# Kernel tuning notes

Measured on AMD Instinct MI355X. Metric: run time of the kernel, lower is better.

Reference implementation:

```python
import jax, jax.numpy as jnp
import numpy as np
from jax.experimental.jet import jet
from jax.experimental.ode import odeint

STATE = 4096
CDIM = 1024
TAY_REG = 2


def sol_recursive(order, f, z, t):
    """Higher-order derivatives of the ODE dynamics via Taylor-mode (jet)."""
    if order < 2:
        return f(z, t), jnp.zeros_like(z)
    z_shape = z.shape
    z_t = jnp.concatenate((jnp.ravel(z), jnp.array([t], dtype=z.dtype)))

    def g(z_t):
        zz, tt = jnp.reshape(z_t[:-1], z_shape), z_t[-1]
        dz = jnp.ravel(f(zz, tt))
        dt = jnp.array([1.0], dtype=z_t.dtype)
        return jnp.concatenate((dz, dt))

    y0, yns = jet(g, (z_t,), ((jnp.ones_like(z_t),),))
    for _ in range(order - 1):
        y0, yns = jet(g, (z_t,), ((y0, *yns),))
    return jnp.reshape(y0[:-1], z_shape), jnp.reshape(yns[-2][:-1], z_shape)


def augment_dynamics(reg, dynamics):
    def aug_dynamics(yr, t):
        y, r = yr
        dydt, dy_r = sol_recursive(reg, dynamics, y, t)
        return dydt, jnp.mean(dy_r ** 2)[None] * jnp.ones(1, y.dtype) if False else (dydt, jnp.mean(dy_r ** 2) * jnp.ones(1, y.dtype))
    # flatten conditional artifact: redefine cleanly
    def aug(yr, t):
        y, r = yr
        dydt, dy_r = sol_recursive(reg, dynamics, y, t)
        return dydt, jnp.mean(dy_r ** 2) * jnp.ones(1, y.dtype)
    return aug


def setup_inputs() -> dict:
    key = jax.random.key(0)
    ks = jax.random.split(key, 5)
    fan_in = CDIM + STATE + 1
    s = 0.5 / np.sqrt(fan_in)  # tame Lipschitz constant -> modest adaptive step count
    h = jax.random.normal(ks[0], (STATE,), dtype=jnp.float32)
    c = jax.random.normal(ks[1], (CDIM,), dtype=jnp.float32)
    t = jnp.float32(1.0)
    W1 = jax.random.normal(ks[2], (fan_in, STATE), dtype=jnp.float32) * s
    b1 = jnp.zeros((STATE,), dtype=jnp.float32)
    W2 = jax.random.normal(ks[3], (fan_in, STATE), dtype=jnp.float32) * s
    b2 = jnp.zeros((STATE,), dtype=jnp.float32)
    return {"h": h, "t": t, "c": c, "W1": W1, "b1": b1, "W2": W2, "b2": b2}


def reference(h, t, c, W1, b1, W2, b2):
    # MLPDynamics: sigmoid(h) -> hstack(c, ., t) -> lin1 -> sigmoid -> hstack(c, ., t) -> lin2
    def dyn(hh, tt):
        out = jax.nn.sigmoid(hh)
        x = jnp.hstack((c, out, tt))          # [CDIM+STATE+1]
        out = jax.nn.sigmoid(x @ W1 + b1)     # [STATE]
        x2 = jnp.hstack((c, out, tt))
        return x2 @ W2 + b2                   # [STATE]

    aug = augment_dynamics(TAY_REG, dyn)
    ts = jnp.stack([jnp.zeros_like(t), t])
    ys, rs = odeint(aug, (h, jnp.zeros(1, h.dtype)), ts)
    # jnp.split(., 2)[1].squeeze() over the 2-row time axis == take row 1
    h1 = ys[1]
    r1 = rs[1].squeeze()
    return (h1, r1)
```

## Files before the change

kernel.cpp:

```cpp
#include <hip/hip_runtime.h>

#define N      4096
#define NROWS  4097
#define NC     1024
#define STEPS  4
#define TPB    256

typedef unsigned short us8 __attribute__((ext_vector_type(8)));

__device__ __forceinline__ float bf2f(unsigned short u) {
  union { unsigned int i; float f; } v; v.i = ((unsigned int)u) << 16; return v.f;
}
__device__ __forceinline__ unsigned short f2bf(float f) {
  union { float f; unsigned int i; } v; v.f = f;
  const unsigned int u = v.i;
  return (unsigned short)((u + 0x7FFFu + ((u >> 16) & 1u)) >> 16);
}
__device__ __forceinline__ float sigf(float x) { return 1.0f / (1.0f + __expf(-x)); }

__global__ __launch_bounds__(TPB) void k_init(const float* __restrict__ h,
                                              const float* __restrict__ b1,
                                              const float* __restrict__ b2,
                                              float* __restrict__ ycur,
                                              float* __restrict__ cp1,
                                              float* __restrict__ cp2,
                                              float* __restrict__ rk) {
  const int j = blockIdx.x * TPB + threadIdx.x;
  if (j < N) { ycur[j] = h[j]; cp1[j] = b1[j]; cp2[j] = b2[j]; }
  if (j < 16) rk[j] = 0.f;
}

__global__ __launch_bounds__(TPB) void k_conv(const float* __restrict__ W1,
                                              const float* __restrict__ W2,
                                              unsigned short* __restrict__ W1bf,
                                              unsigned short* __restrict__ W2bf) {
  const int row = blockIdx.x;
  const float* __restrict__ src = (blockIdx.y ? W2 : W1) + (size_t)(NC + row) * N;
  unsigned short* __restrict__ dst = (blockIdx.y ? W2bf : W1bf) + (size_t)row * N;
#pragma unroll
  for (int it = 0; it < 2; ++it) {
    const int col = it * 2048 + threadIdx.x * 8;
    const float4 a = *reinterpret_cast<const float4*>(src + col);
    const float4 b = *reinterpret_cast<const float4*>(src + col + 4);
    us8 o;
    o[0] = f2bf(a.x); o[1] = f2bf(a.y); o[2] = f2bf(a.z); o[3] = f2bf(a.w);
    o[4] = f2bf(b.x); o[5] = f2bf(b.y); o[6] = f2bf(b.z); o[7] = f2bf(b.w);
    *reinterpret_cast<us8*>(dst + col) = o;
  }
}

__global__ __launch_bounds__(TPB) void k_cpart(const float* __restrict__ W1,
                                               const float* __restrict__ W2,
                                               const float* __restrict__ c,
                                               float* __restrict__ cp1,
                                               float* __restrict__ cp2) {
  const float* __restrict__ W = blockIdx.z ? W2 : W1;
  float* __restrict__ cp = blockIdx.z ? cp2 : cp1;
  __shared__ float xs[128];
  __shared__ float red[8][256];
  const int tid = threadIdx.x;
  const int cb = blockIdx.x, rc = blockIdx.y;
  const int r0 = rc * 128;
  if (tid < 128) xs[tid] = c[r0 + tid];
  __syncthreads();
  const int cg = tid & 31, rg = tid >> 5;
  const float* __restrict__ wbase = W + (size_t)r0 * N + cb * 256 + cg * 8;
  float a[8] = {0,0,0,0,0,0,0,0};
#pragma unroll
  for (int k = 0; k < 16; ++k) {
    const int r = rg + (k << 3);
    const float xv = xs[r];
    const float4 wa = *reinterpret_cast<const float4*>(wbase + (size_t)r * N);
    const float4 wb = *reinterpret_cast<const float4*>(wbase + (size_t)r * N + 4);
    a[0] = fmaf(wa.x, xv, a[0]); a[1] = fmaf(wa.y, xv, a[1]);
    a[2] = fmaf(wa.z, xv, a[2]); a[3] = fmaf(wa.w, xv, a[3]);
    a[4] = fmaf(wb.x, xv, a[4]); a[5] = fmaf(wb.y, xv, a[5]);
    a[6] = fmaf(wb.z, xv, a[6]); a[7] = fmaf(wb.w, xv, a[7]);
  }
#pragma unroll
  for (int e = 0; e < 8; ++e) red[rg][cg * 8 + e] = a[e];
  __syncthreads();
  float ssum = 0.f;
#pragma unroll
  for (int g = 0; g < 8; ++g) ssum += red[g][tid];
  atomicAdd(&cp[cb * 256 + tid], ssum);
}

__global__ __launch_bounds__(TPB) void k_phase(
    int mode,
    const unsigned short* __restrict__ Wbf,
    const float* __restrict__ part_in,
    float* __restrict__ part_out,
    const float* __restrict__ cpart,
    const float* __restrict__ tptr,
    float* __restrict__ u1,
    float* __restrict__ fcur,
    const float* __restrict__ fprev,
    float* __restrict__ ycur,
    float* __restrict__ ksum,
    float* __restrict__ rk,
    int rkIdx, int s, float csv, float tmul, float tadd) {
  __shared__ float xs[128];
  __shared__ float red[8][256];
  const int tid = threadIdx.x;
  const int cb = blockIdx.x, rc = blockIdx.y;
  const int j0 = rc * 128;
  const float dtv = tptr[0] * (1.0f / STEPS);

  if (tid < 128) {
    const int j = j0 + tid;
    float xv;
    if (mode == 0) {
      xv = sigf(ycur[j]);
    } else {
      float ssum = 0.f;
#pragma unroll 8
      for (int r = 0; r < 32; ++r) ssum += part_in[(r << 12) + j];
      if (mode == 1) {
        const float u = ssum + cpart[j];
        if (cb == 0) u1[j] = u;
        xv = sigf(u);
      } else if (mode == 2) {
        const float fv = ssum + cpart[j];
        if (cb == 0) fcur[j] = fv;
        float ys = ycur[j];
        if (csv != 0.f) ys = fmaf(csv * dtv, fprev[j], ys);
        const float s0 = sigf(ys);
        xv = s0 * (1.f - s0) * fv;
      } else if (mode == 3) {
        if (cb == 0) {
          const float fc = fcur[j];
          if (s == 0)      ksum[j] = fc;
          else if (s < 3)  ksum[j] = fmaf(2.f, fc, ksum[j]);
          else             ycur[j] = fmaf(dtv * (1.f / 6.f), ksum[j] + fc, ycur[j]);
        }
        const float s1 = sigf(u1[j]);
        xv = s1 * (1.f - s1) * ssum;
      } else {
        float v = ssum * ssum;
#pragma unroll
        for (int off = 32; off >= 1; off >>= 1) v += __shfl_down(v, off);
        if (cb == 0 && (tid & 63) == 0) atomicAdd(&rk[rkIdx], v);
        float ys = ycur[j];
        if (csv != 0.f) ys = fmaf(csv * dtv, fprev[j], ys);
        xv = sigf(ys);
      }
    }
    xs[tid] = xv;
  }
  __syncthreads();

  const int cg = tid & 31, rg = tid >> 5;
  const unsigned short* __restrict__ wbase =
      Wbf + (size_t)j0 * N + cb * 256 + cg * 8;
  float a[8] = {0,0,0,0,0,0,0,0};
#pragma unroll
  for (int k = 0; k < 16; ++k) {
    const int r = rg + (k << 3);
    const float xv = xs[r];
    const us8 w = *reinterpret_cast<const us8*>(wbase + (size_t)r * N);
#pragma unroll
    for (int e = 0; e < 8; ++e) a[e] = fmaf(bf2f(w[e]), xv, a[e]);
  }
  if (rc == 31 && rg == 0) {
    const float coef = fmaf(tmul, dtv, tadd);
    const us8 w = *reinterpret_cast<const us8*>(
        Wbf + (size_t)N * N + cb * 256 + cg * 8);
#pragma unroll
    for (int e = 0; e < 8; ++e) a[e] = fmaf(bf2f(w[e]), coef, a[e]);
  }
#pragma unroll
  for (int e = 0; e < 8; ++e) red[rg][cg * 8 + e] = a[e];
  __syncthreads();
  float ssum = 0.f;
#pragma unroll
  for (int g = 0; g < 8; ++g) ssum += red[g][tid];
  part_out[(rc << 12) + cb * 256 + tid] = ssum;
}

__global__ __launch_bounds__(128) void k_last(const float* __restrict__ part_in,
                                              const float* __restrict__ ycur,
                                              float* __restrict__ rk,
                                              float* __restrict__ out) {
  const int tid = threadIdx.x;
  const int j = blockIdx.x * 128 + tid;
  float df = 0.f;
#pragma unroll 8
  for (int r = 0; r < 32; ++r) df += part_in[(r << 12) + j];
  float v = df * df;
#pragma unroll
  for (int off = 32; off >= 1; off >>= 1) v += __shfl_down(v, off);
  if ((tid & 63) == 0) atomicAdd(&rk[15], v);
  out[j] = ycur[j];
}

__global__ void k_out(const float* __restrict__ rk, const float* __restrict__ tptr,
                      float* __restrict__ out) {
  if (threadIdx.x == 0) {
    const float dtv = tptr[0] * (1.0f / STEPS);
    float r = 0.f;
    for (int st = 0; st < STEPS; ++st)
      r += rk[4 * st] + 2.f * rk[4 * st + 1] + 2.f * rk[4 * st + 2] + rk[4 * st + 3];
    out[N] = r * (dtv / 6.f) * (1.0f / N);
  }
}

extern "C" void kernel_launch(void* const* d_in, const int* in_sizes, int n_in,
                              void* d_out, int out_size, void* d_ws, size_t ws_size,
                              hipStream_t stream) {
  const float* h  = (const float*)d_in[0];
  const float* t  = (const float*)d_in[1];
  const float* c  = (const float*)d_in[2];
  const float* W1 = (const float*)d_in[3];
  const float* b1 = (const float*)d_in[4];
  const float* W2 = (const float*)d_in[5];
  const float* b2 = (const float*)d_in[6];
  float* out = (float*)d_out;

  char* ws = (char*)d_ws;
  const size_t wb = (size_t)NROWS * N * sizeof(unsigned short);
  unsigned short* W1bf = (unsigned short*)ws;
  unsigned short* W2bf = (unsigned short*)(ws + wb);
  float* fp = (float*)(ws + 2 * wb);
  float* partA = fp;
  float* partB = partA + 32 * N;
  float* cp1   = partB + 32 * N;
  float* cp2   = cp1 + N;
  float* u1    = cp2 + N;
  float* fb0   = u1 + N;
  float* fb1   = fb0 + N;
  float* ycur  = fb1 + N;
  float* ksum  = ycur + N;
  float* rk    = ksum + N;

  k_init<<<16, TPB, 0, stream>>>(h, b1, b2, ycur, cp1, cp2, rk);
  k_conv<<<dim3(NROWS, 2), TPB, 0, stream>>>(W1, W2, W1bf, W2bf);
  k_cpart<<<dim3(16, 8, 2), TPB, 0, stream>>>(W1, W2, c, cp1, cp2);

  const float csv[4] = {0.f, 0.5f, 0.5f, 1.f};
  float* bufs[2] = {partA, partB};
  int flip = 0;
  for (int i = 0; i < 16; ++i) {
    const int step = i >> 2, s = i & 3;
    const float tsv = (float)step + csv[s];
    float* fcur  = (i & 1) ? fb1 : fb0;
    float* fprev = (i & 1) ? fb0 : fb1;

    {
      float* po = bufs[flip]; const float* pi = bufs[flip ^ 1]; flip ^= 1;
      if (i == 0)
        k_phase<<<dim3(16, 32), TPB, 0, stream>>>(0, W1bf, pi, po, cp1, t,
            u1, fcur, fprev, ycur, ksum, rk, 0, s, 0.f, 0.f, 0.f);
      else
        k_phase<<<dim3(16, 32), TPB, 0, stream>>>(4, W1bf, pi, po, cp1, t,
            u1, fcur, fprev, ycur, ksum, rk, i - 1, s, csv[s], tsv, 0.f);
    }
    {
      float* po = bufs[flip]; const float* pi = bufs[flip ^ 1]; flip ^= 1;
      k_phase<<<dim3(16, 32), TPB, 0, stream>>>(1, W2bf, pi, po, cp1, t,
          u1, fcur, fprev, ycur, ksum, rk, 0, s, csv[s], tsv, 0.f);
    }
    {
      float* po = bufs[flip]; const float* pi = bufs[flip ^ 1]; flip ^= 1;
      k_phase<<<dim3(16, 32), TPB, 0, stream>>>(2, W1bf, pi, po, cp2, t,
          u1, fcur, fprev, ycur, ksum, rk, 0, s, csv[s], 0.f, 1.f);
    }
    {
      float* po = bufs[flip]; const float* pi = bufs[flip ^ 1]; flip ^= 1;
      k_phase<<<dim3(16, 32), TPB, 0, stream>>>(3, W2bf, pi, po, cp2, t,
          u1, fcur, fprev, ycur, ksum, rk, 0, s, csv[s], 0.f, 1.f);
    }
  }
  k_last<<<32, 128, 0, stream>>>(bufs[flip ^ 1], ycur, rk, out);
  k_out<<<1, 64, 0, stream>>>(rk, t, out);
}
```

Measured before the change: 851.2 us.

## Transpose weights so each block computes full dot products without split-K partials

```diff
diff --git a/kernel.cpp b/kernel.cpp
--- a/kernel.cpp
+++ b/kernel.cpp
@@ -1,10 +1,10 @@
 #include <hip/hip_runtime.h>
 
 #define N      4096
-#define NROWS  4097
 #define NC     1024
 #define STEPS  4
 #define TPB    256
+#define NBLK   512
 
 typedef unsigned short us8 __attribute__((ext_vector_type(8)));
 
@@ -19,33 +19,49 @@
 __device__ __forceinline__ float sigf(float x) { return 1.0f / (1.0f + __expf(-x)); }
 
 __global__ __launch_bounds__(TPB) void k_init(const float* __restrict__ h,
+                                              const float* __restrict__ W1,
+                                              const float* __restrict__ W2,
                                               const float* __restrict__ b1,
                                               const float* __restrict__ b2,
                                               float* __restrict__ ycur,
                                               float* __restrict__ cp1,
                                               float* __restrict__ cp2,
+                                              float* __restrict__ xA,
+                                              float* __restrict__ T1,
+                                              float* __restrict__ T2,
                                               float* __restrict__ rk) {
   const int j = blockIdx.x * TPB + threadIdx.x;
-  if (j < N) { ycur[j] = h[j]; cp1[j] = b1[j]; cp2[j] = b2[j]; }
+  if (j < N) {
+    ycur[j] = h[j];
+    cp1[j] = b1[j];
+    cp2[j] = b2[j];
+    xA[j] = sigf(h[j]);
+    T1[j] = W1[(size_t)(NC + N) * N + j];
+    T2[j] = W2[(size_t)(NC + N) * N + j];
+  }
   if (j < 16) rk[j] = 0.f;
 }
 
 __global__ __launch_bounds__(TPB) void k_conv(const float* __restrict__ W1,
                                               const float* __restrict__ W2,
-                                              unsigned short* __restrict__ W1bf,
-                                              unsigned short* __restrict__ W2bf) {
-  const int row = blockIdx.x;
-  const float* __restrict__ src = (blockIdx.y ? W2 : W1) + (size_t)(NC + row) * N;
-  unsigned short* __restrict__ dst = (blockIdx.y ? W2bf : W1bf) + (size_t)row * N;
-#pragma unroll
-  for (int it = 0; it < 2; ++it) {
-    const int col = it * 2048 + threadIdx.x * 8;
-    const float4 a = *reinterpret_cast<const float4*>(src + col);
-    const float4 b = *reinterpret_cast<const float4*>(src + col + 4);
-    us8 o;
-    o[0] = f2bf(a.x); o[1] = f2bf(a.y); o[2] = f2bf(a.z); o[3] = f2bf(a.w);
-    o[4] = f2bf(b.x); o[5] = f2bf(b.y); o[6] = f2bf(b.z); o[7] = f2bf(b.w);
-    *reinterpret_cast<us8*>(dst + col) = o;
+                                              unsigned short* __restrict__ Wt1,
+                                              unsigned short* __restrict__ Wt2) {
+  __shared__ float tile[64][65];
+  const float* __restrict__ W = blockIdx.z ? W2 : W1;
+  unsigned short* __restrict__ Wt = blockIdx.z ? Wt2 : Wt1;
+  const int i0 = blockIdx.x * 64;
+  const int j0 = blockIdx.y * 64;
+  const int c = threadIdx.x & 63, rq = threadIdx.x >> 6;
+#pragma unroll
+  for (int m = 0; m < 16; ++m) {
+    const int ii = (m << 2) + rq;
+    tile[ii][c] = W[(size_t)(NC + i0 + ii) * N + j0 + c];
+  }
+  __syncthreads();
+#pragma unroll
+  for (int m = 0; m < 16; ++m) {
+    const int jj = (m << 2) + rq;
+    Wt[(size_t)(j0 + jj) * N + i0 + c] = f2bf(tile[c][jj]);
   }
 }
 
@@ -88,120 +104,100 @@
 
 __global__ __launch_bounds__(TPB) void k_phase(
     int mode,
-    const unsigned short* __restrict__ Wbf,
-    const float* __restrict__ part_in,
-    float* __restrict__ part_out,
-    const float* __restrict__ cpart,
+    const unsigned short* __restrict__ Wt,
+    const float* __restrict__ T,
+    const float* __restrict__ cp,
+    const float* __restrict__ xin,
+    float* __restrict__ xout,
+    float* __restrict__ fbuf,
     const float* __restrict__ tptr,
-    float* __restrict__ u1,
-    float* __restrict__ fcur,
-    const float* __restrict__ fprev,
     float* __restrict__ ycur,
     float* __restrict__ ksum,
     float* __restrict__ rk,
-    int rkIdx, int s, float csv, float tmul, float tadd) {
-  __shared__ float xs[128];
-  __shared__ float red[8][256];
+    int rkIdx, int s, float csvn, float tA, float tB) {
+  __shared__ float xs[N];
+  __shared__ float red[4];
   const int tid = threadIdx.x;
-  const int cb = blockIdx.x, rc = blockIdx.y;
-  const int j0 = rc * 128;
-  const float dtv = tptr[0] * (1.0f / STEPS);
-
-  if (tid < 128) {
-    const int j = j0 + tid;
-    float xv;
-    if (mode == 0) {
-      xv = sigf(ycur[j]);
-    } else {
-      float ssum = 0.f;
-#pragma unroll 8
-      for (int r = 0; r < 32; ++r) ssum += part_in[(r << 12) + j];
-      if (mode == 1) {
-        const float u = ssum + cpart[j];
-        if (cb == 0) u1[j] = u;
-        xv = sigf(u);
+#pragma unroll
+  for (int q = 0; q < 4; ++q)
+    reinterpret_cast<float4*>(xs)[q * 256 + tid] =
+        reinterpret_cast<const float4*>(xin)[q * 256 + tid];
+  __syncthreads();
+
+  const int w = tid >> 6, l = tid & 63;
+  const int j0 = blockIdx.x * 8 + w * 2;
+  const unsigned short* __restrict__ w0 = Wt + (size_t)j0 * N;
+  const unsigned short* __restrict__ w1 = w0 + N;
+  float a0 = 0.f, a1 = 0.f;
+#pragma unroll
+  for (int p = 0; p < 8; ++p) {
+    const int off = (p << 9) + (l << 3);
+    const us8 wa = *reinterpret_cast<const us8*>(w0 + off);
+    const us8 wb = *reinterpret_cast<const us8*>(w1 + off);
+    const float* xp = xs + off;
+#pragma unroll
+    for (int e = 0; e < 8; ++e) {
+      a0 = fmaf(bf2f(wa[e]), xp[e], a0);
+      a1 = fmaf(bf2f(wb[e]), xp[e], a1);
+    }
+  }
+#pragma unroll
+  for (int o = 32; o >= 1; o >>= 1) {
+    a0 += __shfl_down(a0, o);
+    a1 += __shfl_down(a1, o);
+  }
+
+  if (l == 0) {
+    const float dt = tptr[0] * (1.0f / STEPS);
+    const float tcoef = fmaf(tA, dt, tB);
+    float v = 0.f;
+    float dots[2] = {a0, a1};
+#pragma unroll
+    for (int e = 0; e < 2; ++e) {
+      const int j = j0 + e;
+      const float a = fmaf(tcoef, T[j], dots[e]);
+      if (mode == 0) {
+        xout[j] = sigf(a + cp[j]);
+      } else if (mode == 1) {
+        const float fv = a + cp[j];
+        fbuf[j] = fv;
+        const float s0 = xout[j];
+        xout[j] = s0 * (1.f - s0) * fv;
       } else if (mode == 2) {
-        const float fv = ssum + cpart[j];
-        if (cb == 0) fcur[j] = fv;
-        float ys = ycur[j];
-        if (csv != 0.f) ys = fmaf(csv * dtv, fprev[j], ys);
-        const float s0 = sigf(ys);
-        xv = s0 * (1.f - s0) * fv;
-      } else if (mode == 3) {
-        if (cb == 0) {
-          const float fc = fcur[j];
-          if (s == 0)      ksum[j] = fc;
-          else if (s < 3)  ksum[j] = fmaf(2.f, fc, ksum[j]);
-          else             ycur[j] = fmaf(dtv * (1.f / 6.f), ksum[j] + fc, ycur[j]);
-        }
-        const float s1 = sigf(u1[j]);
-        xv = s1 * (1.f - s1) * ssum;
+        const float s1 = xout[j];
+        xout[j] = s1 * (1.f - s1) * a;
       } else {
-        float v = ssum * ssum;
-#pragma unroll
-        for (int off = 32; off >= 1; off >>= 1) v += __shfl_down(v, off);
-        if (cb == 0 && (tid & 63) == 0) atomicAdd(&rk[rkIdx], v);
-        float ys = ycur[j];
-        if (csv != 0.f) ys = fmaf(csv * dtv, fprev[j], ys);
-        xv = sigf(ys);
+        v += a * a;
+        const float fc = fbuf[j];
+        float y = ycur[j];
+        if (s == 0)      ksum[j] = fc;
+        else if (s < 3)  ksum[j] = fmaf(2.f, fc, ksum[j]);
+        else { y = fmaf(dt * (1.f / 6.f), ksum[j] + fc, y); ycur[j] = y; }
+        xout[j] = sigf(fmaf(csvn * dt, fc, y));
       }
     }
-    xs[tid] = xv;
-  }
-  __syncthreads();
-
-  const int cg = tid & 31, rg = tid >> 5;
-  const unsigned short* __restrict__ wbase =
-      Wbf + (size_t)j0 * N + cb * 256 + cg * 8;
-  float a[8] = {0,0,0,0,0,0,0,0};
-#pragma unroll
-  for (int k = 0; k < 16; ++k) {
-    const int r = rg + (k << 3);
-    const float xv = xs[r];
-    const us8 w = *reinterpret_cast<const us8*>(wbase + (size_t)r * N);
-#pragma unroll
-    for (int e = 0; e < 8; ++e) a[e] = fmaf(bf2f(w[e]), xv, a[e]);
-  }
-  if (rc == 31 && rg == 0) {
-    const float coef = fmaf(tmul, dtv, tadd);
-    const us8 w = *reinterpret_cast<const us8*>(
-        Wbf + (size_t)N * N + cb * 256 + cg * 8);
-#pragma unroll
-    for (int e = 0; e < 8; ++e) a[e] = fmaf(bf2f(w[e]), coef, a[e]);
-  }
-#pragma unroll
-  for (int e = 0; e < 8; ++e) red[rg][cg * 8 + e] = a[e];
-  __syncthreads();
-  float ssum = 0.f;
-#pragma unroll
-  for (int g = 0; g < 8; ++g) ssum += red[g][tid];
-  part_out[(rc << 12) + cb * 256 + tid] = ssum;
-}
-
-__global__ __launch_bounds__(128) void k_last(const float* __restrict__ part_in,
-                                              const float* __restrict__ ycur,
-                                              float* __restrict__ rk,
-                                              float* __restrict__ out) {
-  const int tid = threadIdx.x;
-  const int j = blockIdx.x * 128 + tid;
-  float df = 0.f;
-#pragma unroll 8
-  for (int r = 0; r < 32; ++r) df += part_in[(r << 12) + j];
-  float v = df * df;
-#pragma unroll
-  for (int off = 32; off >= 1; off >>= 1) v += __shfl_down(v, off);
-  if ((tid & 63) == 0) atomicAdd(&rk[15], v);
+    if (mode == 3) red[w] = v;
+  }
+  if (mode == 3) {
+    __syncthreads();
+    if (tid == 0) atomicAdd(&rk[rkIdx], red[0] + red[1] + red[2] + red[3]);
+  }
+}
+
+__global__ __launch_bounds__(128) void k_fin(const float* __restrict__ ycur,
+                                             float* __restrict__ out) {
+  const int j = blockIdx.x * 128 + threadIdx.x;
   out[j] = ycur[j];
 }
 
 __global__ void k_out(const float* __restrict__ rk, const float* __restrict__ tptr,
                       float* __restrict__ out) {
   if (threadIdx.x == 0) {
-    const float dtv = tptr[0] * (1.0f / STEPS);
+    const float dt = tptr[0] * (1.0f / STEPS);
     float r = 0.f;
     for (int st = 0; st < STEPS; ++st)
       r += rk[4 * st] + 2.f * rk[4 * st + 1] + 2.f * rk[4 * st + 2] + rk[4 * st + 3];
-    out[N] = r * (dtv / 6.f) * (1.0f / N);
+    out[N] = r * (dt / 6.f) * (1.0f / N);
   }
 }
 
@@ -218,59 +214,45 @@
   float* out = (float*)d_out;
 
   char* ws = (char*)d_ws;
-  const size_t wb = (size_t)NROWS * N * sizeof(unsigned short);
-  unsigned short* W1bf = (unsigned short*)ws;
-  unsigned short* W2bf = (unsigned short*)(ws + wb);
+  const size_t wb = (size_t)N * N * sizeof(unsigned short);
+  unsigned short* Wt1 = (unsigned short*)ws;
+  unsigned short* Wt2 = (unsigned short*)(ws + wb);
   float* fp = (float*)(ws + 2 * wb);
-  float* partA = fp;
-  float* partB = partA + 32 * N;
-  float* cp1   = partB + 32 * N;
-  float* cp2   = cp1 + N;
-  float* u1    = cp2 + N;
-  float* fb0   = u1 + N;
-  float* fb1   = fb0 + N;
-  float* ycur  = fb1 + N;
-  float* ksum  = ycur + N;
-  float* rk    = ksum + N;
-
-  k_init<<<16, TPB, 0, stream>>>(h, b1, b2, ycur, cp1, cp2, rk);
-  k_conv<<<dim3(NROWS, 2), TPB, 0, stream>>>(W1, W2, W1bf, W2bf);
+  float* xA   = fp;
+  float* xB   = xA + N;
+  float* cp1  = xB + N;
+  float* cp2  = cp1 + N;
+  float* fbuf = cp2 + N;
+  float* ycur = fbuf + N;
+  float* ksum = ycur + N;
+  float* T1   = ksum + N;
+  float* T2   = T1 + N;
+  float* rk   = T2 + N;
+
+  k_init<<<16, TPB, 0, stream>>>(h, W1, W2, b1, b2, ycur, cp1, cp2, xA, T1, T2, rk);
+  k_conv<<<dim3(64, 64, 2), TPB, 0, stream>>>(W1, W2, Wt1, Wt2);
   k_cpart<<<dim3(16, 8, 2), TPB, 0, stream>>>(W1, W2, c, cp1, cp2);
 
   const float csv[4] = {0.f, 0.5f, 0.5f, 1.f};
-  float* bufs[2] = {partA, partB};
-  int flip = 0;
+  float* xb[2] = {xA, xB};
+  int xp = 0;
   for (int i = 0; i < 16; ++i) {
     const int step = i >> 2, s = i & 3;
     const float tsv = (float)step + csv[s];
-    float* fcur  = (i & 1) ? fb1 : fb0;
-    float* fprev = (i & 1) ? fb0 : fb1;
-
-    {
-      float* po = bufs[flip]; const float* pi = bufs[flip ^ 1]; flip ^= 1;
-      if (i == 0)
-        k_phase<<<dim3(16, 32), TPB, 0, stream>>>(0, W1bf, pi, po, cp1, t,
-            u1, fcur, fprev, ycur, ksum, rk, 0, s, 0.f, 0.f, 0.f);
-      else
-        k_phase<<<dim3(16, 32), TPB, 0, stream>>>(4, W1bf, pi, po, cp1, t,
-            u1, fcur, fprev, ycur, ksum, rk, i - 1, s, csv[s], tsv, 0.f);
-    }
-    {
-      float* po = bufs[flip]; const float* pi = bufs[flip ^ 1]; flip ^= 1;
-      k_phase<<<dim3(16, 32), TPB, 0, stream>>>(1, W2bf, pi, po, cp1, t,
-          u1, fcur, fprev, ycur, ksum, rk, 0, s, csv[s], tsv, 0.f);
-    }
-    {
-      float* po = bufs[flip]; const float* pi = bufs[flip ^ 1]; flip ^= 1;
-      k_phase<<<dim3(16, 32), TPB, 0, stream>>>(2, W1bf, pi, po, cp2, t,
-          u1, fcur, fprev, ycur, ksum, rk, 0, s, csv[s], 0.f, 1.f);
-    }
-    {
-      float* po = bufs[flip]; const float* pi = bufs[flip ^ 1]; flip ^= 1;
-      k_phase<<<dim3(16, 32), TPB, 0, stream>>>(3, W2bf, pi, po, cp2, t,
-          u1, fcur, fprev, ycur, ksum, rk, 0, s, csv[s], 0.f, 1.f);
-    }
-  }
-  k_last<<<32, 128, 0, stream>>>(bufs[flip ^ 1], ycur, rk, out);
+    k_phase<<<NBLK, TPB, 0, stream>>>(0, Wt1, T1, cp1, xb[xp], xb[xp ^ 1], fbuf,
+                                      t, ycur, ksum, rk, 0, s, 0.f, tsv, 0.f);
+    xp ^= 1;
+    k_phase<<<NBLK, TPB, 0, stream>>>(1, Wt2, T2, cp2, xb[xp], xb[xp ^ 1], fbuf,
+                                      t, ycur, ksum, rk, 0, s, 0.f, tsv, 0.f);
+    xp ^= 1;
+    k_phase<<<NBLK, TPB, 0, stream>>>(2, Wt1, T1, nullptr, xb[xp], xb[xp ^ 1], fbuf,
+                                      t, ycur, ksum, rk, 0, s, 0.f, 0.f, 1.f);
+    xp ^= 1;
+    k_phase<<<NBLK, TPB, 0, stream>>>(3, Wt2, T2, nullptr, xb[xp], xb[xp ^ 1], fbuf,
+                                      t, ycur, ksum, rk, i, s, csv[(s + 1) & 3],
+                                      0.f, 1.f);
+    xp ^= 1;
+  }
+  k_fin<<<32, 128, 0, stream>>>(ycur, out);
   k_out<<<1, 64, 0, stream>>>(rk, t, out);
 }
```

Result: no change. 863.2 us (+1.4%).
